# Kernel optimization log

Hardware: AMD Instinct MI355X
Metric: run time of the kernel (lower is better)

The kernel has to match this reference:

```python
import jax, jax.numpy as jnp
import numpy as np

SEQ_LEN = 2048
HIDDEN = 4096


def setup_inputs() -> dict:
    key = jax.random.key(0)
    ks = jax.random.split(key, 12)
    H = HIDDEN
    s = 1.0 / np.sqrt(H)  # xavier-ish scale
    return {
        "input_sequence": jax.random.normal(ks[0], (SEQ_LEN,), dtype=jnp.float32),
        "horizon": 64,
        "u_Wx": jax.random.normal(ks[1], (H, 1), dtype=jnp.float32) * s,
        "u_Wh": jax.random.normal(ks[2], (H, H), dtype=jnp.float32) * s,
        "u_b": jax.random.normal(ks[3], (H, 1), dtype=jnp.float32) * s,
        "r_Wx": jax.random.normal(ks[4], (H, 1), dtype=jnp.float32) * s,
        "r_Wh": jax.random.normal(ks[5], (H, H), dtype=jnp.float32) * s,
        "r_b": jax.random.normal(ks[6], (H, 1), dtype=jnp.float32) * s,
        "Wx": jax.random.normal(ks[7], (H, 1), dtype=jnp.float32) * s,
        "Wh": jax.random.normal(ks[8], (H, H), dtype=jnp.float32) * s,
        "b": jax.random.normal(ks[9], (H, 1), dtype=jnp.float32) * s,
        "V": jax.random.normal(ks[10], (1, H), dtype=jnp.float32) * s,
        "c": jax.random.normal(ks[11], (1, 1), dtype=jnp.float32) * s,
    }


def reference(input_sequence, horizon, u_Wx, u_Wh, u_b, r_Wx, r_Wh, r_b, Wx, Wh, b, V, c):
    # hidden state kept as [H] vector; weights kept in original [H,1]/[H,H] layout.
    uwx, ub = u_Wx[:, 0], u_b[:, 0]
    rwx, rb = r_Wx[:, 0], r_b[:, 0]
    wx, bb = Wx[:, 0], b[:, 0]
    v, c0 = V[0], c[0, 0]

    def cell(h, x):
        # x: scalar input; h: [H]
        u = jax.nn.sigmoid(uwx * x + u_Wh @ h + ub)
        r = jax.nn.sigmoid(rwx * x + r_Wh @ h + rb)
        h_hat = jnp.tanh(wx * x + r * (Wh @ h) + bb)
        h_new = (1.0 - u) * h + u * h_hat
        y = v @ h_new + c0  # scalar output
        return h_new, y

    h0 = jnp.zeros((HIDDEN,), dtype=input_sequence.dtype)
    # Phase 1: consume the input sequence
    h1, ys = jax.lax.scan(cell, h0, input_sequence)
    y_last = ys[-1]

    def ar_step(carry, _):
        h, y_prev = carry
        h_new, y = cell(h, y_prev)
        return (h_new, y), y

    _, preds = jax.lax.scan(ar_step, (h1, y_last), None, length=horizon)
    return preds  # [horizon], equals outputs.view(-1)[-horizon:]
```

## Files before the change

kernel.cpp:

```cpp
#include <hip/hip_runtime.h>
#include <hip/hip_cooperative_groups.h>
#include <hip/hip_fp16.h>
#include <math.h>

namespace cg = cooperative_groups;

#define H      4096
#define SEQ    2048
#define HOR    64
#define NBLK   256
#define NTHR   512
#define NWAVE  (NTHR / 64)
#define RPW    2
#define J      16

#define NREP       8
#define LINE_F     32
#define REP_F      (NBLK * LINE_F)
#define BUF_F      (NREP * REP_F)

#define SMEM_H     (H * 4)
#define SMEM_R     (NWAVE * RPW * H * 2)
#define SMEM_HH    (H * 2)
#define SMEM_RED   128
#define SMEM_BYTES (SMEM_H + SMEM_R + SMEM_HH + SMEM_RED)

typedef float f32x4_t __attribute__((ext_vector_type(4)));
typedef _Float16 h2_t __attribute__((ext_vector_type(2)));

__device__ __forceinline__ h2_t as_h2(unsigned u) {
    union { unsigned u; h2_t h; } c; c.u = u; return c.h;
}

__device__ __forceinline__ void store_l3_f4(float* p, float a, float b, float c, float d) {
    f32x4_t w;
    w.x = a; w.y = b; w.z = c; w.w = d;
    asm volatile("global_store_dwordx4 %0, %1, off sc0 sc1"
                 :: "v"(p), "v"(w) : "memory");
}
__device__ __forceinline__ float4 load_l3_f4(const float4* p) {
    float4 v;
    asm volatile("global_load_dwordx4 %0, %1, off sc0 sc1"
                 : "=v"(v) : "v"(p) : "memory");
    return v;
}
__device__ __forceinline__ void vm_drain() {
    asm volatile("s_waitcnt vmcnt(0)" ::: "memory");
}

__device__ __forceinline__ float wave_reduce(float v) {
#pragma unroll
    for (int o = 32; o > 0; o >>= 1) v += __shfl_xor(v, o, 64);
    return v;
}

__device__ __forceinline__ float dot4(float4 a, float4 b) {
    float s = a.x * b.x;
    s = fmaf(a.y, b.y, s);
    s = fmaf(a.z, b.z, s);
    s = fmaf(a.w, b.w, s);
    return s;
}

union H4U { uint2 u; __half h[4]; };

__device__ __forceinline__ uint2 pack4(float4 v) {
    H4U c;
    c.h[0] = __float2half_rn(v.x); c.h[1] = __float2half_rn(v.y);
    c.h[2] = __float2half_rn(v.z); c.h[3] = __float2half_rn(v.w);
    return c.u;
}

__global__ __launch_bounds__(NTHR, 1) void gru_kernel(
    const float* __restrict__ xseq,
    const float* __restrict__ uWx, const float* __restrict__ uWh, const float* __restrict__ ubv,
    const float* __restrict__ rWx, const float* __restrict__ rWh, const float* __restrict__ rbv,
    const float* __restrict__ wxv, const float* __restrict__ Whm, const float* __restrict__ bbv,
    const float* __restrict__ Vv,  const float* __restrict__ cv,
    float* __restrict__ out, float* __restrict__ ws)
{
    cg::grid_group grid = cg::this_grid();
    extern __shared__ unsigned char smem[];
    float* hF  = (float*)smem;
    uint4* rWm = (uint4*)(smem + SMEM_H);
    uint2* hH2 = (uint2*)(smem + SMEM_H + SMEM_R);
    float* red = (float*)(smem + SMEM_H + SMEM_R + SMEM_HH);
    float* pub = red + NWAVE;
    int*   cnt = (int*)(pub + NWAVE * RPW);

    const int tid  = threadIdx.x;
    const int wv   = tid >> 6;
    const int lane = tid & 63;
    const int bid  = blockIdx.x;
    const int r0   = bid * (NWAVE * RPW) + wv * RPW;
    const int r1   = r0 + 1;

    float* hA = ws;
    float* hB = ws + BUF_F;

    if (tid == 0) *cnt = 0;

    const float4* w0p = (const float4*)(Whm + (size_t)r0 * H);
    const float4* w1p = (const float4*)(Whm + (size_t)r1 * H);
    const float4* u0p = (const float4*)(uWh + (size_t)r0 * H);
    const float4* u1p = (const float4*)(uWh + (size_t)r1 * H);
    const float4* p0p = (const float4*)(rWh + (size_t)r0 * H);
    const float4* p1p = (const float4*)(rWh + (size_t)r1 * H);

    uint2  wpA[J], wpB[J];
    uint2  uA[J], uB[J];
    uint4* rsm = rWm + wv * (H / 4);

#pragma unroll
    for (int j = 0; j < J; ++j) {
        const int idx = j * 64 + lane;
        wpA[j] = pack4(w0p[idx]);
        wpB[j] = pack4(w1p[idx]);
        uA[j]  = pack4(u0p[idx]);
        uB[j]  = pack4(u1p[idx]);
        const uint2 a = pack4(p0p[idx]);
        const uint2 b = pack4(p1p[idx]);
        rsm[idx] = make_uint4(a.x, a.y, b.x, b.y);
    }
#pragma unroll
    for (int j = 0; j < J; ++j) {
        asm volatile("" : "+v"(wpA[j].x), "+v"(wpA[j].y));
        asm volatile("" : "+v"(wpB[j].x), "+v"(wpB[j].y));
        asm volatile("" : "+v"(uA[j].x), "+v"(uA[j].y));
        asm volatile("" : "+v"(uB[j].x), "+v"(uB[j].y));
    }

    const float uwx0 = uWx[r0], uwx1 = uWx[r1], ub0 = ubv[r0], ub1 = ubv[r1];
    const float rwx0 = rWx[r0], rwx1 = rWx[r1], rb0 = rbv[r0], rb1 = rbv[r1];
    const float wx0  = wxv[r0], wx1  = wxv[r1], bb0 = bbv[r0], bb1 = bbv[r1];
    const float c0 = cv[0];

    const int prep = lane >> 3, psub = lane & 7;
    const int pub_off = prep * REP_F + bid * LINE_F + psub * 4;
    const int gslot = wv * 32 + (lane >> 1);
    const int ghalf = lane & 1;
    const int gat_off = (bid & (NREP - 1)) * REP_F + gslot * LINE_F + ghalf * 16;
    const int hf4 = gslot * 4 + ghalf * 2;

    if (wv == 0)
        store_l3_f4(hA + pub_off, 0.f, 0.f, 0.f, 0.f);

    grid.sync();

    const float4* v4g = (const float4*)Vv;
    const float4* hF4 = (const float4*)hF;

#pragma unroll 1
    for (int t = 0; t < SEQ + HOR; ++t) {
        const float* hin  = (t & 1) ? hB : hA;
        float*       hout = (t & 1) ? hA : hB;
        const float tagf  = (float)t;
        const float tagf1 = (float)(t + 1);

        const float4* src = (const float4*)(hin + gat_off);
        float4 q0, q1, q2, q3;
        int bk = 0;
        for (;;) {
            q0 = load_l3_f4(src);
            q1 = load_l3_f4(src + 1);
            q2 = load_l3_f4(src + 2);
            q3 = load_l3_f4(src + 3);
            vm_drain();
            const float mn = fminf(fminf(fminf(q0.y, q0.w), fminf(q1.y, q1.w)),
                                   fminf(fminf(q2.y, q2.w), fminf(q3.y, q3.w)));
            if (mn >= tagf) break;
            if      (bk == 0) { bk = 1; }
            else if (bk == 1) { __builtin_amdgcn_s_sleep(1); bk = 2; }
            else if (bk == 2) { __builtin_amdgcn_s_sleep(2); bk = 3; }
            else if (bk == 3) { __builtin_amdgcn_s_sleep(4); bk = 4; }
            else              { __builtin_amdgcn_s_sleep(8); }
        }
        const float4 sa = make_float4(q0.x, q0.z, q1.x, q1.z);
        const float4 sb = make_float4(q2.x, q2.z, q3.x, q3.z);
        ((float4*)hF)[hf4]     = sa;
        ((float4*)hF)[hf4 + 1] = sb;
        const uint2 pa = pack4(sa), pb = pack4(sb);
        ((uint4*)hH2)[hf4 >> 1] = make_uint4(pa.x, pa.y, pb.x, pb.y);
        __syncthreads();

        float x;
        if (t < SEQ) {
            x = xseq[t];
        } else {
            float4 a0 = hF4[tid];
            float4 a1 = hF4[tid + NTHR];
            float p = dot4(a0, v4g[tid]) + dot4(a1, v4g[tid + NTHR]);
            p = wave_reduce(p);
            if (lane == 0) red[wv] = p;
            __syncthreads();
            float y = c0;
#pragma unroll
            for (int w = 0; w < NWAVE; ++w) y += red[w];
            x = y;
            if (t > SEQ && bid == 0 && tid == 0) out[t - SEQ - 1] = y;
        }

        float au0 = 0.f, au1 = 0.f, ar0 = 0.f, ar1 = 0.f, aw0 = 0.f, aw1 = 0.f;
#pragma unroll
        for (int j = 0; j < J; ++j) {
            const int idx = j * 64 + lane;
            const uint2  hh = hH2[idx];
            aw0 = __builtin_amdgcn_fdot2(as_h2(wpA[j].x), as_h2(hh.x), aw0, false);
            aw0 = __builtin_amdgcn_fdot2(as_h2(wpA[j].y), as_h2(hh.y), aw0, false);
            aw1 = __builtin_amdgcn_fdot2(as_h2(wpB[j].x), as_h2(hh.x), aw1, false);
            aw1 = __builtin_amdgcn_fdot2(as_h2(wpB[j].y), as_h2(hh.y), aw1, false);
            au0 = __builtin_amdgcn_fdot2(as_h2(uA[j].x), as_h2(hh.x), au0, false);
            au0 = __builtin_amdgcn_fdot2(as_h2(uA[j].y), as_h2(hh.y), au0, false);
            au1 = __builtin_amdgcn_fdot2(as_h2(uB[j].x), as_h2(hh.x), au1, false);
            au1 = __builtin_amdgcn_fdot2(as_h2(uB[j].y), as_h2(hh.y), au1, false);
            const uint4 m = rsm[idx];
            ar0 = __builtin_amdgcn_fdot2(as_h2(m.x), as_h2(hh.x), ar0, false);
            ar0 = __builtin_amdgcn_fdot2(as_h2(m.y), as_h2(hh.y), ar0, false);
            ar1 = __builtin_amdgcn_fdot2(as_h2(m.z), as_h2(hh.x), ar1, false);
            ar1 = __builtin_amdgcn_fdot2(as_h2(m.w), as_h2(hh.y), ar1, false);
        }
        au0 = wave_reduce(au0); au1 = wave_reduce(au1);
        ar0 = wave_reduce(ar0); ar1 = wave_reduce(ar1);
        aw0 = wave_reduce(aw0); aw1 = wave_reduce(aw1);

        if (lane < 2) {
            const bool s = (lane == 1);
            const float adu = s ? au1 : au0;
            const float adr = s ? ar1 : ar0;
            const float adw = s ? aw1 : aw0;
            const float uwx = s ? uwx1 : uwx0, ubb = s ? ub1 : ub0;
            const float rwx = s ? rwx1 : rwx0, rbb = s ? rb1 : rb0;
            const float wxx = s ? wx1  : wx0,  bbb = s ? bb1 : bb0;
            const int   rr  = s ? r1 : r0;
            const float ho  = hF[rr];
            const float zu  = fmaf(uwx, x, adu + ubb);
            const float zr  = fmaf(rwx, x, adr + rbb);
            const float u   = 1.f / (1.f + expf(-zu));
            const float g   = 1.f / (1.f + expf(-zr));
            const float hh  = tanhf(fmaf(wxx, x, fmaf(g, adw, bbb)));
            pub[wv * RPW + (s ? 1 : 0)] = fmaf(u, hh - ho, ho);
        }
        asm volatile("s_waitcnt lgkmcnt(0)" ::: "memory");
        int old = 0;
        if (lane == 0) old = atomicAdd(cnt, 1);
        old = __shfl(old, 0, 64);
        if (old == 8 * t + 7) {
            const float h0v = pub[psub * 2], h1v = pub[psub * 2 + 1];
            store_l3_f4(hout + pub_off, h0v, tagf1, h1v, tagf1);
        }
        __syncthreads();
    }

    if (bid == 0) {
        const float tagF = (float)(SEQ + HOR);
        const float4* src = (const float4*)(hA + gat_off);
        float4 q0, q1, q2, q3;
        int bk = 0;
        for (;;) {
            q0 = load_l3_f4(src);
            q1 = load_l3_f4(src + 1);
            q2 = load_l3_f4(src + 2);
            q3 = load_l3_f4(src + 3);
            vm_drain();
            const float mn = fminf(fminf(fminf(q0.y, q0.w), fminf(q1.y, q1.w)),
                                   fminf(fminf(q2.y, q2.w), fminf(q3.y, q3.w)));
            if (mn >= tagF) break;
            if      (bk == 0) { bk = 1; }
            else              { __builtin_amdgcn_s_sleep(2); }
        }
        ((float4*)hF)[hf4]     = make_float4(q0.x, q0.z, q1.x, q1.z);
        ((float4*)hF)[hf4 + 1] = make_float4(q2.x, q2.z, q3.x, q3.z);
        __syncthreads();
        float4 a0 = hF4[tid];
        float4 a1 = hF4[tid + NTHR];
        float p = dot4(a0, v4g[tid]) + dot4(a1, v4g[tid + NTHR]);
        p = wave_reduce(p);
        if (lane == 0) red[wv] = p;
        __syncthreads();
        if (tid == 0) {
            float y = c0;
            for (int w = 0; w < NWAVE; ++w) y += red[w];
            out[HOR - 1] = y;
        }
    }
}

extern "C" void kernel_launch(void* const* d_in, const int* in_sizes, int n_in,
                              void* d_out, int out_size, void* d_ws, size_t ws_size,
                              hipStream_t stream) {
    const float* xseq = (const float*)d_in[0];
    const float* uWx  = (const float*)d_in[2];
    const float* uWh  = (const float*)d_in[3];
    const float* ubv  = (const float*)d_in[4];
    const float* rWx  = (const float*)d_in[5];
    const float* rWh  = (const float*)d_in[6];
    const float* rbv  = (const float*)d_in[7];
    const float* wxv  = (const float*)d_in[8];
    const float* Whm  = (const float*)d_in[9];
    const float* bbv  = (const float*)d_in[10];
    const float* Vv   = (const float*)d_in[11];
    const float* cv   = (const float*)d_in[12];
    float* out = (float*)d_out;
    float* ws  = (float*)d_ws;

    (void)hipFuncSetAttribute((const void*)gru_kernel,
                              hipFuncAttributeMaxDynamicSharedMemorySize, SMEM_BYTES);

    void* args[] = { &xseq, &uWx, &uWh, &ubv, &rWx, &rWh, &rbv,
                     &wxv, &Whm, &bbv, &Vv, &cv, &out, &ws };
    (void)hipLaunchCooperativeKernel((void*)gru_kernel, dim3(NBLK), dim3(NTHR),
                                     args, SMEM_BYTES, stream);
}
```

Measured before the change: 8.759 ms.

## Double-buffer fp16 hidden state in LDS and drop per-step trailing barrier

```diff
diff --git a/kernel.cpp b/kernel.cpp
--- a/kernel.cpp
+++ b/kernel.cpp
@@ -19,11 +19,14 @@
 #define REP_F      (NBLK * LINE_F)
 #define BUF_F      (NREP * REP_F)
 
-#define SMEM_H     (H * 4)
-#define SMEM_R     (NWAVE * RPW * H * 2)
-#define SMEM_HH    (H * 2)
-#define SMEM_RED   128
-#define SMEM_BYTES (SMEM_H + SMEM_R + SMEM_HH + SMEM_RED)
+#define OFF_R      0
+#define OFF_HHA    131072
+#define OFF_HHB    139264
+#define OFF_HOWN   147456
+#define OFF_RED    147520
+#define OFF_PUB    147552
+#define OFF_CNT    147616
+#define SMEM_BYTES 147648
 
 typedef float f32x4_t __attribute__((ext_vector_type(4)));
 typedef _Float16 h2_t __attribute__((ext_vector_type(2)));
@@ -81,12 +84,13 @@
 {
     cg::grid_group grid = cg::this_grid();
     extern __shared__ unsigned char smem[];
-    float* hF  = (float*)smem;
-    uint4* rWm = (uint4*)(smem + SMEM_H);
-    uint2* hH2 = (uint2*)(smem + SMEM_H + SMEM_R);
-    float* red = (float*)(smem + SMEM_H + SMEM_R + SMEM_HH);
-    float* pub = red + NWAVE;
-    int*   cnt = (int*)(pub + NWAVE * RPW);
+    uint4* rWm  = (uint4*)(smem + OFF_R);
+    uint2* hHa  = (uint2*)(smem + OFF_HHA);
+    uint2* hHb  = (uint2*)(smem + OFF_HHB);
+    float* hOwn = (float*)(smem + OFF_HOWN);
+    float* red  = (float*)(smem + OFF_RED);
+    float* pub  = (float*)(smem + OFF_PUB);
+    int*   cnt  = (int*)(smem + OFF_CNT);
 
     const int tid  = threadIdx.x;
     const int wv   = tid >> 6;
@@ -140,7 +144,8 @@
     const int gslot = wv * 32 + (lane >> 1);
     const int ghalf = lane & 1;
     const int gat_off = (bid & (NREP - 1)) * REP_F + gslot * LINE_F + ghalf * 16;
-    const int hf4 = gslot * 4 + ghalf * 2;
+    const int gidx = gslot * 4 + ghalf * 2;
+    const bool own = (wv == (bid >> 5)) && ((lane >> 1) == (bid & 31));
 
     if (wv == 0)
         store_l3_f4(hA + pub_off, 0.f, 0.f, 0.f, 0.f);
@@ -148,7 +153,6 @@
     grid.sync();
 
     const float4* v4g = (const float4*)Vv;
-    const float4* hF4 = (const float4*)hF;
 
 #pragma unroll 1
     for (int t = 0; t < SEQ + HOR; ++t) {
@@ -172,24 +176,25 @@
             if      (bk == 0) { bk = 1; }
             else if (bk == 1) { __builtin_amdgcn_s_sleep(1); bk = 2; }
             else if (bk == 2) { __builtin_amdgcn_s_sleep(2); bk = 3; }
-            else if (bk == 3) { __builtin_amdgcn_s_sleep(4); bk = 4; }
-            else              { __builtin_amdgcn_s_sleep(8); }
+            else              { __builtin_amdgcn_s_sleep(4); }
         }
         const float4 sa = make_float4(q0.x, q0.z, q1.x, q1.z);
         const float4 sb = make_float4(q2.x, q2.z, q3.x, q3.z);
-        ((float4*)hF)[hf4]     = sa;
-        ((float4*)hF)[hf4 + 1] = sb;
         const uint2 pa = pack4(sa), pb = pack4(sb);
-        ((uint4*)hH2)[hf4 >> 1] = make_uint4(pa.x, pa.y, pb.x, pb.y);
+        uint4* hHp4 = (uint4*)((t & 1) ? hHb : hHa);
+        hHp4[gidx >> 1] = make_uint4(pa.x, pa.y, pb.x, pb.y);
+        if (own) {
+            float* hop = hOwn + ghalf * 8;
+            hop[0] = sa.x; hop[1] = sa.y; hop[2] = sa.z; hop[3] = sa.w;
+            hop[4] = sb.x; hop[5] = sb.y; hop[6] = sb.z; hop[7] = sb.w;
+        }
         __syncthreads();
 
         float x;
         if (t < SEQ) {
             x = xseq[t];
         } else {
-            float4 a0 = hF4[tid];
-            float4 a1 = hF4[tid + NTHR];
-            float p = dot4(a0, v4g[tid]) + dot4(a1, v4g[tid + NTHR]);
+            float p = dot4(sa, v4g[gidx]) + dot4(sb, v4g[gidx + 1]);
             p = wave_reduce(p);
             if (lane == 0) red[wv] = p;
             __syncthreads();
@@ -200,11 +205,12 @@
             if (t > SEQ && bid == 0 && tid == 0) out[t - SEQ - 1] = y;
         }
 
+        const uint2* hcur = (t & 1) ? hHb : hHa;
         float au0 = 0.f, au1 = 0.f, ar0 = 0.f, ar1 = 0.f, aw0 = 0.f, aw1 = 0.f;
 #pragma unroll
         for (int j = 0; j < J; ++j) {
             const int idx = j * 64 + lane;
-            const uint2  hh = hH2[idx];
+            const uint2  hh = hcur[idx];
             aw0 = __builtin_amdgcn_fdot2(as_h2(wpA[j].x), as_h2(hh.x), aw0, false);
             aw0 = __builtin_amdgcn_fdot2(as_h2(wpA[j].y), as_h2(hh.y), aw0, false);
             aw1 = __builtin_amdgcn_fdot2(as_h2(wpB[j].x), as_h2(hh.x), aw1, false);
@@ -231,8 +237,7 @@
             const float uwx = s ? uwx1 : uwx0, ubb = s ? ub1 : ub0;
             const float rwx = s ? rwx1 : rwx0, rbb = s ? rb1 : rb0;
             const float wxx = s ? wx1  : wx0,  bbb = s ? bb1 : bb0;
-            const int   rr  = s ? r1 : r0;
-            const float ho  = hF[rr];
+            const float ho  = hOwn[wv * RPW + (s ? 1 : 0)];
             const float zu  = fmaf(uwx, x, adu + ubb);
             const float zr  = fmaf(rwx, x, adr + rbb);
             const float u   = 1.f / (1.f + expf(-zu));
@@ -248,10 +253,10 @@
             const float h0v = pub[psub * 2], h1v = pub[psub * 2 + 1];
             store_l3_f4(hout + pub_off, h0v, tagf1, h1v, tagf1);
         }
+    }
+
+    if (bid == 0) {
         __syncthreads();
-    }
-
-    if (bid == 0) {
         const float tagF = (float)(SEQ + HOR);
         const float4* src = (const float4*)(hA + gat_off);
         float4 q0, q1, q2, q3;
@@ -268,12 +273,9 @@
             if      (bk == 0) { bk = 1; }
             else              { __builtin_amdgcn_s_sleep(2); }
         }
-        ((float4*)hF)[hf4]     = make_float4(q0.x, q0.z, q1.x, q1.z);
-        ((float4*)hF)[hf4 + 1] = make_float4(q2.x, q2.z, q3.x, q3.z);
-        __syncthreads();
-        float4 a0 = hF4[tid];
-        float4 a1 = hF4[tid + NTHR];
-        float p = dot4(a0, v4g[tid]) + dot4(a1, v4g[tid + NTHR]);
+        const float4 sa = make_float4(q0.x, q0.z, q1.x, q1.z);
+        const float4 sb = make_float4(q2.x, q2.z, q3.x, q3.z);
+        float p = dot4(sa, v4g[gidx]) + dot4(sb, v4g[gidx + 1]);
         p = wave_reduce(p);
         if (lane == 0) red[wv] = p;
         __syncthreads();
```

New measurement: 11.20 ms. 27.9% more time.
